# Performance work log

Measured on AMD Instinct MI355X. Metric: run time of the kernel, lower is better.

## Reference

```python
import jax, jax.numpy as jnp
import numpy as np

N_DETS = 16384
DEG = 32
E = N_DETS * DEG
NUM_BLOCKS = 4
SHORTCUT = 128   # shortcutDim
RED = 32         # reducedDim
INNER = 64       # blockInnerDim = 2*32
PW_IN = 9        # pwfeatRawInput
PW_HID = 256     # pwfeatInnerDim
PW_OUT = 32      # pwfeatOutDim


def _xavier(key, shape):
    fan_in, fan_out = shape[-2], shape[-1]
    lim = jnp.sqrt(6.0 / (fan_in + fan_out)).astype(jnp.float32)
    return jax.random.uniform(key, shape, jnp.float32, -lim, lim)


def setup_inputs() -> dict:
    key = jax.random.key(0)
    ks = jax.random.split(key, 24)
    inp = {}
    inp["detFeatures"] = jnp.zeros((N_DETS, SHORTCUT), jnp.float32)
    inp["pairRaw"] = jax.random.normal(ks[0], (E, PW_IN), jnp.float32)
    # every detection has DEG neighbor rows (sorted, all segments non-empty)
    inp["cIdxs"] = jnp.repeat(jnp.arange(N_DETS, dtype=jnp.int32), DEG)
    inp["nIdxs"] = jax.random.randint(ks[1], (E,), 0, N_DETS, jnp.int32)
    # pairwise-feature generator MLP: 9 -> 256 -> 256 -> 32
    inp["g_W1"] = _xavier(ks[2], (PW_IN, PW_HID)); inp["g_b1"] = jnp.zeros((PW_HID,), jnp.float32)
    inp["g_W2"] = _xavier(ks[3], (PW_HID, PW_HID)); inp["g_b2"] = jnp.zeros((PW_HID,), jnp.float32)
    inp["g_W3"] = _xavier(ks[4], (PW_HID, PW_OUT)); inp["g_b3"] = jnp.zeros((PW_OUT,), jnp.float32)
    # per-block params, stacked along leading block dim
    inp["blk_fc1_W"] = _xavier(ks[5], (NUM_BLOCKS, SHORTCUT, RED)); inp["blk_fc1_b"] = jnp.zeros((NUM_BLOCKS, RED), jnp.float32)
    inp["blk_pw_W1"] = _xavier(ks[6], (NUM_BLOCKS, 3 * RED, INNER)); inp["blk_pw_b1"] = jnp.zeros((NUM_BLOCKS, INNER), jnp.float32)
    inp["blk_pw_W2"] = _xavier(ks[7], (NUM_BLOCKS, INNER, INNER)); inp["blk_pw_b2"] = jnp.zeros((NUM_BLOCKS, INNER), jnp.float32)
    inp["blk_post_W1"] = _xavier(ks[8], (NUM_BLOCKS, INNER, INNER)); inp["blk_post_b1"] = jnp.zeros((NUM_BLOCKS, INNER), jnp.float32)
    inp["blk_post_W2"] = _xavier(ks[9], (NUM_BLOCKS, INNER, INNER)); inp["blk_post_b2"] = jnp.zeros((NUM_BLOCKS, INNER), jnp.float32)
    inp["blk_out_W"] = _xavier(ks[10], (NUM_BLOCKS, INNER, SHORTCUT)); inp["blk_out_b"] = jnp.zeros((NUM_BLOCKS, SHORTCUT), jnp.float32)
    inp["s_W"] = _xavier(ks[11], (3, SHORTCUT, SHORTCUT)); inp["s_b"] = jnp.zeros((3, SHORTCUT), jnp.float32)
    inp["pred_W"] = _xavier(ks[12], (SHORTCUT, 1)); inp["pred_b"] = jnp.zeros((1,), jnp.float32)
    return inp


def reference(detFeatures, pairRaw, cIdxs, nIdxs,
              g_W1, g_b1, g_W2, g_b2, g_W3, g_b3,
              blk_fc1_W, blk_fc1_b, blk_pw_W1, blk_pw_b1, blk_pw_W2, blk_pw_b2,
              blk_post_W1, blk_post_b1, blk_post_W2, blk_post_b2,
              blk_out_W, blk_out_b, s_W, s_b, pred_W, pred_b):
    relu = jax.nn.relu
    n_dets = detFeatures.shape[0]
    num_blocks = blk_fc1_W.shape[0]
    # GNet.pairwiseFeaturesFC: pwfeat generator MLP on raw 9-d pair descriptors
    pair = relu(pairRaw @ g_W1 + g_b1)          # (E, 256)
    pair = relu(pair @ g_W2 + g_b2)             # (E, 256)
    pair = relu(pair @ g_W3 + g_b3)             # (E, 32)
    is_id = (cIdxs == nIdxs)[:, None]           # zero-out self-neighbor feats
    x = detFeatures                             # (N, 128)
    for b in range(num_blocks):                 # structurally distinct blocks
        f = relu(x @ blk_fc1_W[b] + blk_fc1_b[b])          # (N, 32)
        cF = f[cIdxs]                                       # (E, 32) gather
        nF = jnp.where(is_id, jnp.float32(0), f[nIdxs])     # (E, 32) gather
        h = jnp.concatenate([pair, cF, nF], axis=1)         # (E, 96)
        h = relu(h @ blk_pw_W1[b] + blk_pw_b1[b])           # (E, 64)
        h = relu(h @ blk_pw_W2[b] + blk_pw_b2[b])           # (E, 64)
        # per-detection max pooling over neighbor rows (segment-max)
        m = jax.ops.segment_max(h, cIdxs, num_segments=n_dets,
                                indices_are_sorted=True)    # (N, 64)
        m = relu(m @ blk_post_W1[b] + blk_post_b1[b])
        m = relu(m @ blk_post_W2[b] + blk_post_b2[b])
        x = relu(x + m @ blk_out_W[b] + blk_out_b[b])        # residual + relu
    for i in range(s_W.shape[0]):
        x = relu(x @ s_W[i] + s_b[i])
    scores = (x @ pred_W + pred_b).reshape(-1)               # (N,)
    return scores
```

## Files before the change

kernel.cpp:

```cpp
#include <hip/hip_runtime.h>

#define N_DETS 16384
#define DEG 32
#define E_EDGES (N_DETS * DEG)
#define EDGE_GRID 512

typedef __attribute__((ext_vector_type(8))) short bf16x8;
typedef __attribute__((ext_vector_type(4))) float f32x4;

__device__ __forceinline__ ushort f32_to_bf16(float v) {
  unsigned u = __float_as_uint(v);
  u += 0x7FFFu + ((u >> 16) & 1u);
  return (ushort)(u >> 16);
}
__device__ __forceinline__ float bf16_to_f32(ushort h) {
  return __uint_as_float((unsigned)h << 16);
}

__global__ __launch_bounds__(256) void split_w_kernel(
    const float* __restrict__ W, ushort* __restrict__ hi, ushort* __restrict__ lo, int N)
{
  const int n = blockIdx.x, k = threadIdx.x;
  const float v = W[(size_t)k * N + n];
  const ushort h = f32_to_bf16(v);
  const ushort l = f32_to_bf16(v - bf16_to_f32(h));
  hi[(size_t)n * 256 + k] = h;
  lo[(size_t)n * 256 + k] = l;
}

__global__ __launch_bounds__(256) void split_edge_w_kernel(
    const float* __restrict__ W1all, const float* __restrict__ W2all,
    ushort* __restrict__ w1h, ushort* __restrict__ w1l,
    ushort* __restrict__ w2h, ushort* __restrict__ w2l)
{
  const int b = blockIdx.x;
  const float* W1 = W1all + b * 6144;
  const float* W2 = W2all + b * 4096;
  for (int i = threadIdx.x; i < 6144; i += 256) {
    const int col = i / 96, k = i % 96;
    const float v = W1[k * 64 + col];
    const ushort h = f32_to_bf16(v);
    w1h[b * 6144 + col * 96 + k] = h;
    w1l[b * 6144 + col * 96 + k] = f32_to_bf16(v - bf16_to_f32(h));
  }
  for (int i = threadIdx.x; i < 4096; i += 256) {
    const int col = i >> 6, k = i & 63;
    const float v = W2[k * 64 + col];
    const ushort h = f32_to_bf16(v);
    w2h[b * 4096 + col * 64 + k] = h;
    w2l[b * 4096 + col * 64 + k] = f32_to_bf16(v - bf16_to_f32(h));
  }
}

__global__ __launch_bounds__(128) void split_score_w_kernel(
    const float* __restrict__ sW, ushort* __restrict__ hi, ushort* __restrict__ lo)
{
  const int layer = blockIdx.x >> 7, col = blockIdx.x & 127, k = threadIdx.x;
  const float v = sW[layer * 16384 + k * 128 + col];
  const ushort h = f32_to_bf16(v);
  hi[layer * 16384 + col * 128 + k] = h;
  lo[layer * 16384 + col * 128 + k] = f32_to_bf16(v - bf16_to_f32(h));
}

__global__ __launch_bounds__(256) void split_post_w_kernel(
    const float* __restrict__ poW1, const float* __restrict__ poW2,
    const float* __restrict__ outW, const float* __restrict__ fc1W,
    ushort* __restrict__ p1h, ushort* __restrict__ p1l,
    ushort* __restrict__ p2h, ushort* __restrict__ p2l,
    ushort* __restrict__ oh,  ushort* __restrict__ ol,
    ushort* __restrict__ fh,  ushort* __restrict__ fl)
{
  const int b = blockIdx.x;
  for (int i = threadIdx.x; i < 4096; i += 256) {
    const int col = i >> 6, k = i & 63;
    float v = poW1[b * 4096 + k * 64 + col];
    ushort h = f32_to_bf16(v);
    p1h[b * 4096 + col * 64 + k] = h;
    p1l[b * 4096 + col * 64 + k] = f32_to_bf16(v - bf16_to_f32(h));
    v = poW2[b * 4096 + k * 64 + col];
    h = f32_to_bf16(v);
    p2h[b * 4096 + col * 64 + k] = h;
    p2l[b * 4096 + col * 64 + k] = f32_to_bf16(v - bf16_to_f32(h));
  }
  for (int i = threadIdx.x; i < 8192; i += 256) {
    const int col = i >> 6, k = i & 63;
    const float v = outW[b * 8192 + k * 128 + col];
    const ushort h = f32_to_bf16(v);
    oh[b * 8192 + col * 64 + k] = h;
    ol[b * 8192 + col * 64 + k] = f32_to_bf16(v - bf16_to_f32(h));
  }
  for (int i = threadIdx.x; i < 4096; i += 256) {
    const int col = i >> 7, k = i & 127;
    const float v = fc1W[b * 4096 + k * 32 + col];
    const ushort h = f32_to_bf16(v);
    fh[b * 4096 + col * 128 + k] = h;
    fl[b * 4096 + col * 128 + k] = f32_to_bf16(v - bf16_to_f32(h));
  }
}

#define A_STRIDE 264

__global__ __launch_bounds__(1024, 4) void pair_mlp_kernel(
    const float* __restrict__ raw,
    const float* __restrict__ W1, const float* __restrict__ b1,
    const ushort* __restrict__ w2h, const ushort* __restrict__ w2l,
    const float* __restrict__ b2,
    const ushort* __restrict__ w3h, const ushort* __restrict__ w3l,
    const float* __restrict__ b3,
    ushort* __restrict__ pair_h, ushort* __restrict__ pair_l)
{
  __shared__ __align__(16) ushort ah[64 * A_STRIDE];
  __shared__ __align__(16) ushort al[64 * A_STRIDE];
  __shared__ __align__(16) ushort w3sh[32 * A_STRIDE];
  __shared__ __align__(16) ushort w3sl[32 * A_STRIDE];
  __shared__ __align__(16) float rawt[64 * 12];

  const int t = threadIdx.x;
  const int lane = t & 63, wv = t >> 6;
  const int ln = lane & 15, kg = lane >> 4;

  for (int i = t; i < 32 * 64; i += 1024) {
    const int row = (i * 4) >> 8, col = (i * 4) & 255;
    *(ushort4*)&w3sh[row * A_STRIDE + col] = *(const ushort4*)&w3h[row * 256 + col];
    *(ushort4*)&w3sl[row * A_STRIDE + col] = *(const ushort4*)&w3l[row * 256 + col];
  }

  bf16x8 b2hreg[8], b2lreg[8];
  #pragma unroll
  for (int ks = 0; ks < 8; ++ks) {
    const size_t bo = (size_t)(wv * 16 + ln) * 256 + ks * 32 + kg * 8;
    b2hreg[ks] = *(const bf16x8*)&w2h[bo];
    b2lreg[ks] = *(const bf16x8*)&w2l[bo];
  }
  const float bias2 = b2[wv * 16 + ln];
  const int mt3 = (wv >> 1) & 3, nt3 = wv & 1;
  const float b3v = b3[nt3 * 16 + ln];
  __syncthreads();

  for (int grp = blockIdx.x; grp < E_EDGES / 64; grp += gridDim.x) {
    const long long e0 = (long long)grp * 64;

    if (t < 64 * 9) rawt[(t / 9) * 12 + (t % 9)] = raw[e0 * 9 + t];
    __syncthreads();

    {
      const int col = t & 255, r0 = (t >> 8) * 16;
      const float bv = b1[col];
      float wk[9];
      #pragma unroll
      for (int k = 0; k < 9; ++k) wk[k] = W1[k * 256 + col];
      #pragma unroll
      for (int r = 0; r < 16; ++r) {
        const int row = r0 + r;
        const float4 ra = *(const float4*)&rawt[row * 12];
        const float4 rb = *(const float4*)&rawt[row * 12 + 4];
        const float rc = rawt[row * 12 + 8];
        float s = bv;
        s = fmaf(ra.x, wk[0], s); s = fmaf(ra.y, wk[1], s);
        s = fmaf(ra.z, wk[2], s); s = fmaf(ra.w, wk[3], s);
        s = fmaf(rb.x, wk[4], s); s = fmaf(rb.y, wk[5], s);
        s = fmaf(rb.z, wk[6], s); s = fmaf(rb.w, wk[7], s);
        s = fmaf(rc, wk[8], s);
        const float v = fmaxf(s, 0.f);
        const ushort h = f32_to_bf16(v);
        ah[row * A_STRIDE + col] = h;
        al[row * A_STRIDE + col] = f32_to_bf16(v - bf16_to_f32(h));
      }
    }
    __syncthreads();

    f32x4 acc[4];
    #pragma unroll
    for (int mt = 0; mt < 4; ++mt) {
      acc[mt][0] = 0.f; acc[mt][1] = 0.f; acc[mt][2] = 0.f; acc[mt][3] = 0.f;
    }
    #pragma unroll
    for (int ks = 0; ks < 8; ++ks) {
      const int ka = ks * 32 + kg * 8;
      #pragma unroll
      for (int mt = 0; mt < 4; ++mt) {
        const bf16x8 ahf = *(const bf16x8*)&ah[(mt * 16 + ln) * A_STRIDE + ka];
        const bf16x8 alf = *(const bf16x8*)&al[(mt * 16 + ln) * A_STRIDE + ka];
        acc[mt] = __builtin_amdgcn_mfma_f32_16x16x32_bf16(ahf, b2hreg[ks], acc[mt], 0, 0, 0);
        acc[mt] = __builtin_amdgcn_mfma_f32_16x16x32_bf16(alf, b2hreg[ks], acc[mt], 0, 0, 0);
        acc[mt] = __builtin_amdgcn_mfma_f32_16x16x32_bf16(ahf, b2lreg[ks], acc[mt], 0, 0, 0);
      }
    }
    __syncthreads();

    {
      const int colg = wv * 16 + ln;
      #pragma unroll
      for (int mt = 0; mt < 4; ++mt)
        #pragma unroll
        for (int r = 0; r < 4; ++r) {
          const int rowe = mt * 16 + kg * 4 + r;
          const float v = fmaxf(acc[mt][r] + bias2, 0.f);
          const ushort h = f32_to_bf16(v);
          ah[rowe * A_STRIDE + colg] = h;
          al[rowe * A_STRIDE + colg] = f32_to_bf16(v - bf16_to_f32(h));
        }
    }
    __syncthreads();

    if (wv < 8) {
      f32x4 acc3;
      acc3[0] = 0.f; acc3[1] = 0.f; acc3[2] = 0.f; acc3[3] = 0.f;
      #pragma unroll
      for (int ks = 0; ks < 8; ++ks) {
        const int ka = ks * 32 + kg * 8;
        const bf16x8 a_h = *(const bf16x8*)&ah[(mt3 * 16 + ln) * A_STRIDE + ka];
        const bf16x8 a_l = *(const bf16x8*)&al[(mt3 * 16 + ln) * A_STRIDE + ka];
        const bf16x8 b_h = *(const bf16x8*)&w3sh[(nt3 * 16 + ln) * A_STRIDE + ka];
        const bf16x8 b_l = *(const bf16x8*)&w3sl[(nt3 * 16 + ln) * A_STRIDE + ka];
        acc3 = __builtin_amdgcn_mfma_f32_16x16x32_bf16(a_h, b_h, acc3, 0, 0, 0);
        acc3 = __builtin_amdgcn_mfma_f32_16x16x32_bf16(a_l, b_h, acc3, 0, 0, 0);
        acc3 = __builtin_amdgcn_mfma_f32_16x16x32_bf16(a_h, b_l, acc3, 0, 0, 0);
      }
      const int col3 = nt3 * 16 + ln;
      #pragma unroll
      for (int r = 0; r < 4; ++r) {
        const int rowe = mt3 * 16 + kg * 4 + r;
        const float v = fmaxf(acc3[r] + b3v, 0.f);
        const ushort h = f32_to_bf16(v);
        const size_t idx = (size_t)(e0 + rowe) * 32 + col3;
        pair_h[idx] = h;
        pair_l[idx] = f32_to_bf16(v - bf16_to_f32(h));
      }
    }
    __syncthreads();
  }
}

__global__ __launch_bounds__(256) void fc1_kernel(
    const float* __restrict__ x, const float* __restrict__ W,
    const float* __restrict__ b, float* __restrict__ f,
    ushort* __restrict__ f_h, ushort* __restrict__ f_l)
{
  __shared__ float Wl[128 * 32];
  const int t = threadIdx.x;
  #pragma unroll
  for (int j = 0; j < 4; ++j) {
    const int off = t * 4 + j * 1024;
    *(float4*)&Wl[off] = *(const float4*)&W[off];
  }
  __syncthreads();
  const int c = t & 31, rr = t >> 5;
  const long long r = (long long)blockIdx.x * 8 + rr;
  const float* xr = x + r * 128;
  float acc = b[c];
  #pragma unroll 8
  for (int k = 0; k < 128; k += 4) {
    const float4 a = *(const float4*)&xr[k];
    acc = fmaf(a.x, Wl[(k + 0) * 32 + c], acc);
    acc = fmaf(a.y, Wl[(k + 1) * 32 + c], acc);
    acc = fmaf(a.z, Wl[(k + 2) * 32 + c], acc);
    acc = fmaf(a.w, Wl[(k + 3) * 32 + c], acc);
  }
  const float v = fmaxf(acc, 0.f);
  f[r * 32 + c] = v;
  const ushort h = f32_to_bf16(v);
  f_h[r * 32 + c] = h;
  f_l[r * 32 + c] = f32_to_bf16(v - bf16_to_f32(h));
}

#define W1S 104
#define W2S 72
#define CTS 36

__global__ __launch_bounds__(512, 2) void edge_kernel(
    const ushort* __restrict__ pair_h, const ushort* __restrict__ pair_l,
    const float* __restrict__ f,
    const ushort* __restrict__ f_h, const ushort* __restrict__ f_l,
    const int* __restrict__ nIdxs,
    const float* __restrict__ W1g, const float* __restrict__ bb1,
    const ushort* __restrict__ gw1h, const ushort* __restrict__ gw1l,
    const ushort* __restrict__ gw2h, const ushort* __restrict__ gw2l,
    const float* __restrict__ bb2,
    float* __restrict__ m)
{
  __shared__ __align__(16) ushort W1hS[64 * W1S], W1lS[64 * W1S];
  __shared__ __align__(16) ushort W2hS[64 * W2S], W2lS[64 * W2S];
  __shared__ __align__(16) float  W1cT[64 * CTS];
  __shared__ __align__(16) ushort h1h[8][32 * W2S], h1l[8][32 * W2S];

  const int t = threadIdx.x;
  const int lane = t & 63, wv = t >> 6;
  const int ln = lane & 15, kg = lane >> 4;

  for (int i = t; i < 1536; i += 512) {
    const int idx = i * 4, row = idx / 96, k = idx % 96;
    *(ushort4*)&W1hS[row * W1S + k] = *(const ushort4*)&gw1h[idx];
    *(ushort4*)&W1lS[row * W1S + k] = *(const ushort4*)&gw1l[idx];
  }
  for (int i = t; i < 1024; i += 512) {
    const int idx = i * 4, row = idx >> 6, k = idx & 63;
    *(ushort4*)&W2hS[row * W2S + k] = *(const ushort4*)&gw2h[idx];
    *(ushort4*)&W2lS[row * W2S + k] = *(const ushort4*)&gw2l[idx];
  }
  for (int i = t; i < 2048; i += 512) {
    const int col = i >> 5, j = i & 31;
    W1cT[col * CTS + j] = W1g[(32 + j) * 64 + col];
  }
  __syncthreads();

  for (int dg = blockIdx.x; dg < N_DETS / 8; dg += gridDim.x) {
    const int d = dg * 8 + wv;
    const long long e0 = (long long)d * 32;

    float cfs[4];
    {
      const float4 fv0 = *(const float4*)&f[(size_t)d * 32 + kg * 8];
      const float4 fv1 = *(const float4*)&f[(size_t)d * 32 + kg * 8 + 4];
      #pragma unroll
      for (int nt = 0; nt < 4; ++nt) {
        const int col = nt * 16 + ln;
        const float4 w0 = *(const float4*)&W1cT[col * CTS + kg * 8];
        const float4 w1 = *(const float4*)&W1cT[col * CTS + kg * 8 + 4];
        float s = fv0.x * w0.x + fv0.y * w0.y + fv0.z * w0.z + fv0.w * w0.w
                + fv1.x * w1.x + fv1.y * w1.y + fv1.z * w1.z + fv1.w * w1.w;
        s += __shfl_xor(s, 16);
        s += __shfl_xor(s, 32);
        cfs[nt] = s + bb1[col];
      }
    }

    f32x4 acc1[4][2];
    #pragma unroll
    for (int nt = 0; nt < 4; ++nt)
      #pragma unroll
      for (int mt = 0; mt < 2; ++mt) {
        acc1[nt][mt][0] = 0.f; acc1[nt][mt][1] = 0.f;
        acc1[nt][mt][2] = 0.f; acc1[nt][mt][3] = 0.f;
      }
    bf16x8 ph[2], pl_[2], nh[2], nl_[2];
    #pragma unroll
    for (int mt = 0; mt < 2; ++mt) {
      const long long row = e0 + mt * 16 + ln;
      ph[mt]  = *(const bf16x8*)&pair_h[row * 32 + kg * 8];
      pl_[mt] = *(const bf16x8*)&pair_l[row * 32 + kg * 8];
      const int n = nIdxs[row];
      bf16x8 vh = *(const bf16x8*)&f_h[(size_t)n * 32 + kg * 8];
      bf16x8 vl = *(const bf16x8*)&f_l[(size_t)n * 32 + kg * 8];
      if (n == d) { vh = (bf16x8){0,0,0,0,0,0,0,0}; vl = (bf16x8){0,0,0,0,0,0,0,0}; }
      nh[mt] = vh; nl_[mt] = vl;
    }
    #pragma unroll
    for (int nt = 0; nt < 4; ++nt) {
      const int bro = (nt * 16 + ln) * W1S;
      const bf16x8 b0h = *(const bf16x8*)&W1hS[bro + kg * 8];
      const bf16x8 b0l = *(const bf16x8*)&W1lS[bro + kg * 8];
      const bf16x8 b1h = *(const bf16x8*)&W1hS[bro + 64 + kg * 8];
      const bf16x8 b1l = *(const bf16x8*)&W1lS[bro + 64 + kg * 8];
      #pragma unroll
      for (int mt = 0; mt < 2; ++mt) {
        acc1[nt][mt] = __builtin_amdgcn_mfma_f32_16x16x32_bf16(ph[mt], b0h, acc1[nt][mt], 0, 0, 0);
        acc1[nt][mt] = __builtin_amdgcn_mfma_f32_16x16x32_bf16(pl_[mt], b0h, acc1[nt][mt], 0, 0, 0);
        acc1[nt][mt] = __builtin_amdgcn_mfma_f32_16x16x32_bf16(ph[mt], b0l, acc1[nt][mt], 0, 0, 0);
        acc1[nt][mt] = __builtin_amdgcn_mfma_f32_16x16x32_bf16(nh[mt], b1h, acc1[nt][mt], 0, 0, 0);
        acc1[nt][mt] = __builtin_amdgcn_mfma_f32_16x16x32_bf16(nl_[mt], b1h, acc1[nt][mt], 0, 0, 0);
        acc1[nt][mt] = __builtin_amdgcn_mfma_f32_16x16x32_bf16(nh[mt], b1l, acc1[nt][mt], 0, 0, 0);
      }
    }

    #pragma unroll
    for (int nt = 0; nt < 4; ++nt) {
      const int col = nt * 16 + ln;
      #pragma unroll
      for (int mt = 0; mt < 2; ++mt)
        #pragma unroll
        for (int r = 0; r < 4; ++r) {
          const int row = mt * 16 + kg * 4 + r;
          const float v = fmaxf(acc1[nt][mt][r] + cfs[nt], 0.f);
          const ushort h = f32_to_bf16(v);
          h1h[wv][row * W2S + col] = h;
          h1l[wv][row * W2S + col] = f32_to_bf16(v - bf16_to_f32(h));
        }
    }

    f32x4 acc2[4][2];
    #pragma unroll
    for (int mt = 0; mt < 4; ++mt)
      #pragma unroll
      for (int nt = 0; nt < 2; ++nt) {
        acc2[mt][nt][0] = 0.f; acc2[mt][nt][1] = 0.f;
        acc2[mt][nt][2] = 0.f; acc2[mt][nt][3] = 0.f;
      }
    #pragma unroll
    for (int ks = 0; ks < 2; ++ks) {
      const int ka = ks * 32 + kg * 8;
      bf16x8 bh[2], bl[2];
      #pragma unroll
      for (int nt = 0; nt < 2; ++nt) {
        bh[nt] = *(const bf16x8*)&h1h[wv][(nt * 16 + ln) * W2S + ka];
        bl[nt] = *(const bf16x8*)&h1l[wv][(nt * 16 + ln) * W2S + ka];
      }
      #pragma unroll
      for (int mt = 0; mt < 4; ++mt) {
        const bf16x8 a_h = *(const bf16x8*)&W2hS[(mt * 16 + ln) * W2S + ka];
        const bf16x8 a_l = *(const bf16x8*)&W2lS[(mt * 16 + ln) * W2S + ka];
        #pragma unroll
        for (int nt = 0; nt < 2; ++nt) {
          acc2[mt][nt] = __builtin_amdgcn_mfma_f32_16x16x32_bf16(a_h, bh[nt], acc2[mt][nt], 0, 0, 0);
          acc2[mt][nt] = __builtin_amdgcn_mfma_f32_16x16x32_bf16(a_h, bl[nt], acc2[mt][nt], 0, 0, 0);
          acc2[mt][nt] = __builtin_amdgcn_mfma_f32_16x16x32_bf16(a_l, bh[nt], acc2[mt][nt], 0, 0, 0);
        }
      }
    }

    #pragma unroll
    for (int mt = 0; mt < 4; ++mt)
      #pragma unroll
      for (int r = 0; r < 4; ++r) {
        float mx = fmaxf(acc2[mt][0][r], acc2[mt][1][r]);
        mx = fmaxf(mx, __shfl_xor(mx, 1));
        mx = fmaxf(mx, __shfl_xor(mx, 2));
        mx = fmaxf(mx, __shfl_xor(mx, 4));
        mx = fmaxf(mx, __shfl_xor(mx, 8));
        if (ln == mt * 4 + r) {
          const int outcol = mt * 16 + kg * 4 + r;
          m[(size_t)d * 64 + outcol] = fmaxf(mx + bb2[outcol], 0.f);
        }
      }
  }
}

#define PS 72
#define PXS 136

__global__ __launch_bounds__(512) void postfc1_kernel(
    const float* __restrict__ m, const float* __restrict__ x,
    const ushort* __restrict__ p1h, const ushort* __restrict__ p1l,
    const float* __restrict__ pob1,
    const ushort* __restrict__ p2h, const ushort* __restrict__ p2l,
    const float* __restrict__ pob2,
    const ushort* __restrict__ oh, const ushort* __restrict__ ol,
    const float* __restrict__ outb,
    const ushort* __restrict__ fch, const ushort* __restrict__ fcl,
    const float* __restrict__ fcb, int do_fc1,
    float* __restrict__ y,
    float* __restrict__ f, ushort* __restrict__ f_h, ushort* __restrict__ f_l)
{
  __shared__ __align__(16) ushort mh[32 * PS], ml[32 * PS];
  __shared__ __align__(16) ushort hh[32 * PS], hl[32 * PS];
  __shared__ __align__(16) ushort yh[32 * PXS], yl[32 * PXS];
  const int t = threadIdx.x;
  const int lane = t & 63, wv = t >> 6;
  const int ln = lane & 15, kg = lane >> 4;
  const long long r0 = (long long)blockIdx.x * 32;

  for (int i = t; i < 32 * 16; i += 512) {
    const int row = i >> 4, cq = (i & 15) * 4;
    const float4 v4 = *(const float4*)&m[(r0 + row) * 64 + cq];
    const float vv[4] = {v4.x, v4.y, v4.z, v4.w};
    #pragma unroll
    for (int j = 0; j < 4; ++j) {
      const ushort h = f32_to_bf16(vv[j]);
      mh[row * PS + cq + j] = h;
      ml[row * PS + cq + j] = f32_to_bf16(vv[j] - bf16_to_f32(h));
    }
  }
  __syncthreads();

  {
    const int mt = wv >> 2, nt = wv & 3, col = nt * 16 + ln;
    const ushort* bh = p1h + (size_t)col * 64;
    const ushort* bl = p1l + (size_t)col * 64;
    f32x4 acc; acc[0] = 0.f; acc[1] = 0.f; acc[2] = 0.f; acc[3] = 0.f;
    #pragma unroll
    for (int ks = 0; ks < 2; ++ks) {
      const int ka = ks * 32 + kg * 8;
      const bf16x8 a_h = *(const bf16x8*)&mh[(mt * 16 + ln) * PS + ka];
      const bf16x8 a_l = *(const bf16x8*)&ml[(mt * 16 + ln) * PS + ka];
      const bf16x8 b_h = *(const bf16x8*)&bh[ka];
      const bf16x8 b_l = *(const bf16x8*)&bl[ka];
      acc = __builtin_amdgcn_mfma_f32_16x16x32_bf16(a_h, b_h, acc, 0, 0, 0);
      acc = __builtin_amdgcn_mfma_f32_16x16x32_bf16(a_l, b_h, acc, 0, 0, 0);
      acc = __builtin_amdgcn_mfma_f32_16x16x32_bf16(a_h, b_l, acc, 0, 0, 0);
    }
    const float bias = pob1[col];
    #pragma unroll
    for (int r = 0; r < 4; ++r) {
      const int row = mt * 16 + kg * 4 + r;
      const float v = fmaxf(acc[r] + bias, 0.f);
      const ushort h = f32_to_bf16(v);
      hh[row * PS + col] = h;
      hl[row * PS + col] = f32_to_bf16(v - bf16_to_f32(h));
    }
  }
  __syncthreads();

  {
    const int mt = wv >> 2, nt = wv & 3, col = nt * 16 + ln;
    const ushort* bh = p2h + (size_t)col * 64;
    const ushort* bl = p2l + (size_t)col * 64;
    f32x4 acc; acc[0] = 0.f; acc[1] = 0.f; acc[2] = 0.f; acc[3] = 0.f;
    #pragma unroll
    for (int ks = 0; ks < 2; ++ks) {
      const int ka = ks * 32 + kg * 8;
      const bf16x8 a_h = *(const bf16x8*)&hh[(mt * 16 + ln) * PS + ka];
      const bf16x8 a_l = *(const bf16x8*)&hl[(mt * 16 + ln) * PS + ka];
      const bf16x8 b_h = *(const bf16x8*)&bh[ka];
      const bf16x8 b_l = *(const bf16x8*)&bl[ka];
      acc = __builtin_amdgcn_mfma_f32_16x16x32_bf16(a_h, b_h, acc, 0, 0, 0);
      acc = __builtin_amdgcn_mfma_f32_16x16x32_bf16(a_l, b_h, acc, 0, 0, 0);
      acc = __builtin_amdgcn_mfma_f32_16x16x32_bf16(a_h, b_l, acc, 0, 0, 0);
    }
    const float bias = pob2[col];
    __syncthreads();
    #pragma unroll
    for (int r = 0; r < 4; ++r) {
      const int row = mt * 16 + kg * 4 + r;
      const float v = fmaxf(acc[r] + bias, 0.f);
      const ushort h = f32_to_bf16(v);
      mh[row * PS + col] = h;
      ml[row * PS + col] = f32_to_bf16(v - bf16_to_f32(h));
    }
  }
  __syncthreads();

  {
    const int col = wv * 16 + ln;
    const ushort* bh = oh + (size_t)col * 64;
    const ushort* bl = ol + (size_t)col * 64;
    f32x4 acc[2];
    #pragma unroll
    for (int mt = 0; mt < 2; ++mt) {
      acc[mt][0] = 0.f; acc[mt][1] = 0.f; acc[mt][2] = 0.f; acc[mt][3] = 0.f;
    }
    #pragma unroll
    for (int ks = 0; ks < 2; ++ks) {
      const int ka = ks * 32 + kg * 8;
      const bf16x8 b_h = *(const bf16x8*)&bh[ka];
      const bf16x8 b_l = *(const bf16x8*)&bl[ka];
      #pragma unroll
      for (int mt = 0; mt < 2; ++mt) {
        const bf16x8 a_h = *(const bf16x8*)&mh[(mt * 16 + ln) * PS + ka];
        const bf16x8 a_l = *(const bf16x8*)&ml[(mt * 16 + ln) * PS + ka];
        acc[mt] = __builtin_amdgcn_mfma_f32_16x16x32_bf16(a_h, b_h, acc[mt], 0, 0, 0);
        acc[mt] = __builtin_amdgcn_mfma_f32_16x16x32_bf16(a_l, b_h, acc[mt], 0, 0, 0);
        acc[mt] = __builtin_amdgcn_mfma_f32_16x16x32_bf16(a_h, b_l, acc[mt], 0, 0, 0);
      }
    }
    const float bias = outb[col];
    #pragma unroll
    for (int mt = 0; mt < 2; ++mt)
      #pragma unroll
      for (int r = 0; r < 4; ++r) {
        const int row = mt * 16 + kg * 4 + r;
        const size_t idx = (size_t)(r0 + row) * 128 + col;
        const float v = fmaxf(x[idx] + acc[mt][r] + bias, 0.f);
        y[idx] = v;
        const ushort h = f32_to_bf16(v);
        yh[row * PXS + col] = h;
        yl[row * PXS + col] = f32_to_bf16(v - bf16_to_f32(h));
      }
  }
  __syncthreads();

  if (do_fc1 && wv < 4) {
    const int mt = wv >> 1, nt = wv & 1, col = nt * 16 + ln;
    const ushort* bh = fch + (size_t)col * 128;
    const ushort* bl = fcl + (size_t)col * 128;
    f32x4 acc; acc[0] = 0.f; acc[1] = 0.f; acc[2] = 0.f; acc[3] = 0.f;
    #pragma unroll
    for (int ks = 0; ks < 4; ++ks) {
      const int ka = ks * 32 + kg * 8;
      const bf16x8 a_h = *(const bf16x8*)&yh[(mt * 16 + ln) * PXS + ka];
      const bf16x8 a_l = *(const bf16x8*)&yl[(mt * 16 + ln) * PXS + ka];
      const bf16x8 b_h = *(const bf16x8*)&bh[ka];
      const bf16x8 b_l = *(const bf16x8*)&bl[ka];
      acc = __builtin_amdgcn_mfma_f32_16x16x32_bf16(a_h, b_h, acc, 0, 0, 0);
      acc = __builtin_amdgcn_mfma_f32_16x16x32_bf16(a_l, b_h, acc, 0, 0, 0);
      acc = __builtin_amdgcn_mfma_f32_16x16x32_bf16(a_h, b_l, acc, 0, 0, 0);
    }
    const float bias = fcb[col];
    #pragma unroll
    for (int r = 0; r < 4; ++r) {
      const int row = mt * 16 + kg * 4 + r;
      const float v = fmaxf(acc[r] + bias, 0.f);
      const size_t idx = (size_t)(r0 + row) * 32 + col;
      f[idx] = v;
      const ushort h = f32_to_bf16(v);
      f_h[idx] = h;
      f_l[idx] = f32_to_bf16(v - bf16_to_f32(h));
    }
  }
}

#define XS 136

__global__ __launch_bounds__(512) void score_head_kernel(
    const float* __restrict__ x,
    const ushort* __restrict__ swh, const ushort* __restrict__ swl,
    const float* __restrict__ sb,
    const float* __restrict__ pW, const float* __restrict__ pb,
    float* __restrict__ out)
{
  __shared__ __align__(16) ushort xh[2][32 * XS], xl[2][32 * XS];
  __shared__ __align__(16) float hsf[32 * XS];
  __shared__ float pWs[128];
  const int t = threadIdx.x;
  const int lane = t & 63, wv = t >> 6;
  const int ln = lane & 15, kg = lane >> 4;
  const long long r0 = (long long)blockIdx.x * 32;

  if (t < 128) pWs[t] = pW[t];
  for (int i = t; i < 32 * 32; i += 512) {
    const int row = i >> 5, cq = (i & 31) * 4;
    const float4 v4 = *(const float4*)&x[(r0 + row) * 128 + cq];
    const float vv[4] = {v4.x, v4.y, v4.z, v4.w};
    #pragma unroll
    for (int j = 0; j < 4; ++j) {
      const ushort h = f32_to_bf16(vv[j]);
      xh[0][row * XS + cq + j] = h;
      xl[0][row * XS + cq + j] = f32_to_bf16(vv[j] - bf16_to_f32(h));
    }
  }
  __syncthreads();

  const int colg = wv * 16 + ln;
  int cur = 0;
  #pragma unroll 1
  for (int layer = 0; layer < 3; ++layer) {
    const ushort* wh = swh + (size_t)layer * 16384 + (size_t)colg * 128;
    const ushort* wl = swl + (size_t)layer * 16384 + (size_t)colg * 128;
    f32x4 acc[2];
    #pragma unroll
    for (int mt = 0; mt < 2; ++mt) {
      acc[mt][0] = 0.f; acc[mt][1] = 0.f; acc[mt][2] = 0.f; acc[mt][3] = 0.f;
    }
    #pragma unroll
    for (int ks = 0; ks < 4; ++ks) {
      const int ka = ks * 32 + kg * 8;
      const bf16x8 b_h = *(const bf16x8*)&wh[ka];
      const bf16x8 b_l = *(const bf16x8*)&wl[ka];
      #pragma unroll
      for (int mt = 0; mt < 2; ++mt) {
        const bf16x8 a_h = *(const bf16x8*)&xh[cur][(mt * 16 + ln) * XS + ka];
        const bf16x8 a_l = *(const bf16x8*)&xl[cur][(mt * 16 + ln) * XS + ka];
        acc[mt] = __builtin_amdgcn_mfma_f32_16x16x32_bf16(a_h, b_h, acc[mt], 0, 0, 0);
        acc[mt] = __builtin_amdgcn_mfma_f32_16x16x32_bf16(a_l, b_h, acc[mt], 0, 0, 0);
        acc[mt] = __builtin_amdgcn_mfma_f32_16x16x32_bf16(a_h, b_l, acc[mt], 0, 0, 0);
      }
    }
    const float bias = sb[layer * 128 + colg];
    __syncthreads();
    if (layer < 2) {
      #pragma unroll
      for (int mt = 0; mt < 2; ++mt)
        #pragma unroll
        for (int r = 0; r < 4; ++r) {
          const int row = mt * 16 + kg * 4 + r;
          const float v = fmaxf(acc[mt][r] + bias, 0.f);
          const ushort h = f32_to_bf16(v);
          xh[cur ^ 1][row * XS + colg] = h;
          xl[cur ^ 1][row * XS + colg] = f32_to_bf16(v - bf16_to_f32(h));
        }
      cur ^= 1;
    } else {
      #pragma unroll
      for (int mt = 0; mt < 2; ++mt)
        #pragma unroll
        for (int r = 0; r < 4; ++r) {
          const int row = mt * 16 + kg * 4 + r;
          hsf[row * XS + colg] = fmaxf(acc[mt][r] + bias, 0.f);
        }
    }
    __syncthreads();
  }

  {
    const int row = t >> 4, l16 = t & 15;
    const float4 a0 = *(const float4*)&hsf[row * XS + l16 * 8];
    const float4 a1 = *(const float4*)&hsf[row * XS + l16 * 8 + 4];
    const float4 w0 = *(const float4*)&pWs[l16 * 8];
    const float4 w1 = *(const float4*)&pWs[l16 * 8 + 4];
    float s = a0.x * w0.x + a0.y * w0.y + a0.z * w0.z + a0.w * w0.w
            + a1.x * w1.x + a1.y * w1.y + a1.z * w1.z + a1.w * w1.w;
    s += __shfl_xor(s, 1);
    s += __shfl_xor(s, 2);
    s += __shfl_xor(s, 4);
    s += __shfl_xor(s, 8);
    if (l16 == 0) out[r0 + row] = s + pb[0];
  }
}

extern "C" void kernel_launch(void* const* d_in, const int* in_sizes, int n_in,
                              void* d_out, int out_size, void* d_ws, size_t ws_size,
                              hipStream_t stream)
{
  const float* detF    = (const float*)d_in[0];
  const float* pairRaw = (const float*)d_in[1];
  const int*   cIdx    = (const int*)d_in[2];
  const int*   nIdx    = (const int*)d_in[3];
  const float* gW1 = (const float*)d_in[4];   const float* gb1 = (const float*)d_in[5];
  const float* gW2 = (const float*)d_in[6];   const float* gb2 = (const float*)d_in[7];
  const float* gW3 = (const float*)d_in[8];   const float* gb3 = (const float*)d_in[9];
  const float* fc1W = (const float*)d_in[10]; const float* fc1b = (const float*)d_in[11];
  const float* pwW1 = (const float*)d_in[12]; const float* pwb1 = (const float*)d_in[13];
  const float* pwW2 = (const float*)d_in[14]; const float* pwb2 = (const float*)d_in[15];
  const float* poW1 = (const float*)d_in[16]; const float* pob1 = (const float*)d_in[17];
  const float* poW2 = (const float*)d_in[18]; const float* pob2 = (const float*)d_in[19];
  const float* outW = (const float*)d_in[20]; const float* outb = (const float*)d_in[21];
  const float* sW = (const float*)d_in[22];   const float* sb = (const float*)d_in[23];
  const float* predW = (const float*)d_in[24]; const float* predb = (const float*)d_in[25];
  float* out = (float*)d_out;
  (void)cIdx;

  ushort* w2h  = (ushort*)d_ws;
  ushort* w2l  = w2h + 65536;
  ushort* w3h  = w2l + 65536;
  ushort* w3l  = w3h + 8192;
  ushort* w1eh = w3l + 8192;
  ushort* w1el = w1eh + 24576;
  ushort* w2eh = w1el + 24576;
  ushort* w2el = w2eh + 16384;
  ushort* swh  = w2el + 16384;
  ushort* swl  = swh + 49152;
  ushort* p1h  = swl + 49152;
  ushort* p1l  = p1h + 16384;
  ushort* p2h  = p1l + 16384;
  ushort* p2l  = p2h + 16384;
  ushort* ohh  = p2l + 16384;
  ushort* ohl  = ohh + 32768;
  ushort* fth  = ohl + 32768;
  ushort* ftl  = fth + 16384;
  ushort* pair_h = ftl + 16384;
  ushort* pair_l = pair_h + (size_t)E_EDGES * 32;
  ushort* f_h    = pair_l + (size_t)E_EDGES * 32;
  ushort* f_l    = f_h + (size_t)N_DETS * 32;
  float* f  = (float*)(f_l + (size_t)N_DETS * 32);
  float* m  = f  + (size_t)N_DETS * 32;
  float* xa = m  + (size_t)N_DETS * 64;
  float* xb = xa + (size_t)N_DETS * 128;

  hipMemcpyAsync(xa, detF, (size_t)N_DETS * 128 * sizeof(float),
                 hipMemcpyDeviceToDevice, stream);

  split_w_kernel<<<256, 256, 0, stream>>>(gW2, w2h, w2l, 256);
  split_w_kernel<<<32, 256, 0, stream>>>(gW3, w3h, w3l, 32);
  split_edge_w_kernel<<<4, 256, 0, stream>>>(pwW1, pwW2, w1eh, w1el, w2eh, w2el);
  split_score_w_kernel<<<384, 128, 0, stream>>>(sW, swh, swl);
  split_post_w_kernel<<<4, 256, 0, stream>>>(poW1, poW2, outW, fc1W,
      p1h, p1l, p2h, p2l, ohh, ohl, fth, ftl);

  pair_mlp_kernel<<<256, 1024, 0, stream>>>(pairRaw, gW1, gb1,
      w2h, w2l, gb2, w3h, w3l, gb3, pair_h, pair_l);

  fc1_kernel<<<N_DETS / 8, 256, 0, stream>>>(xa, fc1W, fc1b, f, f_h, f_l);

  float* xin = xa;
  float* xout = xb;
  for (int b = 0; b < 4; ++b) {
    edge_kernel<<<EDGE_GRID, 512, 0, stream>>>(pair_h, pair_l, f, f_h, f_l, nIdx,
        pwW1 + b * 6144, pwb1 + b * 64,
        w1eh + b * 6144, w1el + b * 6144, w2eh + b * 4096, w2el + b * 4096,
        pwb2 + b * 64, m);
    const int nb = (b + 1) & 3;
    postfc1_kernel<<<N_DETS / 32, 512, 0, stream>>>(m, xin,
        p1h + b * 4096, p1l + b * 4096, pob1 + b * 64,
        p2h + b * 4096, p2l + b * 4096, pob2 + b * 64,
        ohh + b * 8192, ohl + b * 8192, outb + b * 128,
        fth + nb * 4096, ftl + nb * 4096, fc1b + nb * 32, (b < 3) ? 1 : 0,
        xout, f, f_h, f_l);
    float* tmp = xout; xout = xin; xin = tmp;
  }
  score_head_kernel<<<N_DETS / 32, 512, 0, stream>>>(xin, swh, swl, sb,
      predW, predb, out);
}
```

Baseline: 678.2 us.

## Fuse edge message kernel with post-MLP and next-block fc1 kernel

Merges the per-block edge MLP plus segment-max kernel with the post-MLP, residual and next fc1 kernel into one kernel that handles 32 detections per workgroup. The pooled features stay in shared memory as hi/lo bf16 instead of going through a global fp32 buffer, and one launch per block is dropped. The fc1 output is double-buffered, because neighbor gathers of the current features could otherwise race with writes of the next features. The cost is a large combined LDS footprint that limits occupancy, and a per-tile serialization of the edge and post phases, which removes the old persistent-grid overlap.

```diff
diff --git a/kernel.cpp b/kernel.cpp
--- a/kernel.cpp
+++ b/kernel.cpp
@@ -3,7 +3,6 @@
 #define N_DETS 16384
 #define DEG 32
 #define E_EDGES (N_DETS * DEG)
-#define EDGE_GRID 512
 
 typedef __attribute__((ext_vector_type(8))) short bf16x8;
 typedef __attribute__((ext_vector_type(4))) float f32x4;
@@ -267,8 +266,9 @@
 #define W1S 104
 #define W2S 72
 #define CTS 36
-
-__global__ __launch_bounds__(512, 2) void edge_kernel(
+#define PXS 136
+
+__global__ __launch_bounds__(512, 2) void edge_post_kernel(
     const ushort* __restrict__ pair_h, const ushort* __restrict__ pair_l,
     const float* __restrict__ f,
     const ushort* __restrict__ f_h, const ushort* __restrict__ f_l,
@@ -277,16 +277,37 @@
     const ushort* __restrict__ gw1h, const ushort* __restrict__ gw1l,
     const ushort* __restrict__ gw2h, const ushort* __restrict__ gw2l,
     const float* __restrict__ bb2,
-    float* __restrict__ m)
-{
-  __shared__ __align__(16) ushort W1hS[64 * W1S], W1lS[64 * W1S];
-  __shared__ __align__(16) ushort W2hS[64 * W2S], W2lS[64 * W2S];
-  __shared__ __align__(16) float  W1cT[64 * CTS];
-  __shared__ __align__(16) ushort h1h[8][32 * W2S], h1l[8][32 * W2S];
+    const float* __restrict__ x,
+    const ushort* __restrict__ p1h, const ushort* __restrict__ p1l,
+    const float* __restrict__ pob1,
+    const ushort* __restrict__ p2h, const ushort* __restrict__ p2l,
+    const float* __restrict__ pob2,
+    const ushort* __restrict__ oh, const ushort* __restrict__ ol,
+    const float* __restrict__ outb,
+    const ushort* __restrict__ fch, const ushort* __restrict__ fcl,
+    const float* __restrict__ fcb, int do_fc1,
+    float* __restrict__ y,
+    float* __restrict__ fo, ushort* __restrict__ fo_h, ushort* __restrict__ fo_l)
+{
+  __shared__ __align__(16) unsigned char smem[137216];
+  ushort* W1hS = (ushort*)(smem);
+  ushort* W1lS = (ushort*)(smem + 13312);
+  ushort* W2hS = (ushort*)(smem + 26624);
+  ushort* W2lS = (ushort*)(smem + 35840);
+  float*  W1cT = (float*)(smem + 45056);
+  ushort* msh  = (ushort*)(smem + 54272);
+  ushort* msl  = (ushort*)(smem + 58880);
+  ushort* h1hB = (ushort*)(smem + 63488);
+  ushort* h1lB = (ushort*)(smem + 100352);
+  ushort* hhB  = (ushort*)(smem + 63488);
+  ushort* hlB  = (ushort*)(smem + 68096);
+  ushort* yhB  = (ushort*)(smem + 72704);
+  ushort* ylB  = (ushort*)(smem + 81408);
 
   const int t = threadIdx.x;
   const int lane = t & 63, wv = t >> 6;
   const int ln = lane & 15, kg = lane >> 4;
+  const long long r0 = (long long)blockIdx.x * 32;
 
   for (int i = t; i < 1536; i += 512) {
     const int idx = i * 4, row = idx / 96, k = idx % 96;
@@ -304,9 +325,14 @@
   }
   __syncthreads();
 
-  for (int dg = blockIdx.x; dg < N_DETS / 8; dg += gridDim.x) {
-    const int d = dg * 8 + wv;
+  ushort* h1h = h1hB + wv * 32 * W2S;
+  ushort* h1l = h1lB + wv * 32 * W2S;
+
+  #pragma unroll 1
+  for (int it = 0; it < 4; ++it) {
+    const int d = (int)r0 + it * 8 + wv;
     const long long e0 = (long long)d * 32;
+    const int rowt = it * 8 + wv;
 
     float cfs[4];
     {
@@ -373,8 +399,8 @@
           const int row = mt * 16 + kg * 4 + r;
           const float v = fmaxf(acc1[nt][mt][r] + cfs[nt], 0.f);
           const ushort h = f32_to_bf16(v);
-          h1h[wv][row * W2S + col] = h;
-          h1l[wv][row * W2S + col] = f32_to_bf16(v - bf16_to_f32(h));
+          h1h[row * W2S + col] = h;
+          h1l[row * W2S + col] = f32_to_bf16(v - bf16_to_f32(h));
         }
     }
 
@@ -392,8 +418,8 @@
       bf16x8 bh[2], bl[2];
       #pragma unroll
       for (int nt = 0; nt < 2; ++nt) {
-        bh[nt] = *(const bf16x8*)&h1h[wv][(nt * 16 + ln) * W2S + ka];
-        bl[nt] = *(const bf16x8*)&h1l[wv][(nt * 16 + ln) * W2S + ka];
+        bh[nt] = *(const bf16x8*)&h1h[(nt * 16 + ln) * W2S + ka];
+        bl[nt] = *(const bf16x8*)&h1l[(nt * 16 + ln) * W2S + ka];
       }
       #pragma unroll
       for (int mt = 0; mt < 4; ++mt) {
@@ -419,46 +445,12 @@
         mx = fmaxf(mx, __shfl_xor(mx, 8));
         if (ln == mt * 4 + r) {
           const int outcol = mt * 16 + kg * 4 + r;
-          m[(size_t)d * 64 + outcol] = fmaxf(mx + bb2[outcol], 0.f);
+          const float v = fmaxf(mx + bb2[outcol], 0.f);
+          const ushort h = f32_to_bf16(v);
+          msh[rowt * W2S + outcol] = h;
+          msl[rowt * W2S + outcol] = f32_to_bf16(v - bf16_to_f32(h));
         }
       }
-  }
-}
-
-#define PS 72
-#define PXS 136
-
-__global__ __launch_bounds__(512) void postfc1_kernel(
-    const float* __restrict__ m, const float* __restrict__ x,
-    const ushort* __restrict__ p1h, const ushort* __restrict__ p1l,
-    const float* __restrict__ pob1,
-    const ushort* __restrict__ p2h, const ushort* __restrict__ p2l,
-    const float* __restrict__ pob2,
-    const ushort* __restrict__ oh, const ushort* __restrict__ ol,
-    const float* __restrict__ outb,
-    const ushort* __restrict__ fch, const ushort* __restrict__ fcl,
-    const float* __restrict__ fcb, int do_fc1,
-    float* __restrict__ y,
-    float* __restrict__ f, ushort* __restrict__ f_h, ushort* __restrict__ f_l)
-{
-  __shared__ __align__(16) ushort mh[32 * PS], ml[32 * PS];
-  __shared__ __align__(16) ushort hh[32 * PS], hl[32 * PS];
-  __shared__ __align__(16) ushort yh[32 * PXS], yl[32 * PXS];
-  const int t = threadIdx.x;
-  const int lane = t & 63, wv = t >> 6;
-  const int ln = lane & 15, kg = lane >> 4;
-  const long long r0 = (long long)blockIdx.x * 32;
-
-  for (int i = t; i < 32 * 16; i += 512) {
-    const int row = i >> 4, cq = (i & 15) * 4;
-    const float4 v4 = *(const float4*)&m[(r0 + row) * 64 + cq];
-    const float vv[4] = {v4.x, v4.y, v4.z, v4.w};
-    #pragma unroll
-    for (int j = 0; j < 4; ++j) {
-      const ushort h = f32_to_bf16(vv[j]);
-      mh[row * PS + cq + j] = h;
-      ml[row * PS + cq + j] = f32_to_bf16(vv[j] - bf16_to_f32(h));
-    }
   }
   __syncthreads();
 
@@ -470,8 +462,8 @@
     #pragma unroll
     for (int ks = 0; ks < 2; ++ks) {
       const int ka = ks * 32 + kg * 8;
-      const bf16x8 a_h = *(const bf16x8*)&mh[(mt * 16 + ln) * PS + ka];
-      const bf16x8 a_l = *(const bf16x8*)&ml[(mt * 16 + ln) * PS + ka];
+      const bf16x8 a_h = *(const bf16x8*)&msh[(mt * 16 + ln) * W2S + ka];
+      const bf16x8 a_l = *(const bf16x8*)&msl[(mt * 16 + ln) * W2S + ka];
       const bf16x8 b_h = *(const bf16x8*)&bh[ka];
       const bf16x8 b_l = *(const bf16x8*)&bl[ka];
       acc = __builtin_amdgcn_mfma_f32_16x16x32_bf16(a_h, b_h, acc, 0, 0, 0);
@@ -484,8 +476,8 @@
       const int row = mt * 16 + kg * 4 + r;
       const float v = fmaxf(acc[r] + bias, 0.f);
       const ushort h = f32_to_bf16(v);
-      hh[row * PS + col] = h;
-      hl[row * PS + col] = f32_to_bf16(v - bf16_to_f32(h));
+      hhB[row * W2S + col] = h;
+      hlB[row * W2S + col] = f32_to_bf16(v - bf16_to_f32(h));
     }
   }
   __syncthreads();
@@ -498,8 +490,8 @@
     #pragma unroll
     for (int ks = 0; ks < 2; ++ks) {
       const int ka = ks * 32 + kg * 8;
-      const bf16x8 a_h = *(const bf16x8*)&hh[(mt * 16 + ln) * PS + ka];
-      const bf16x8 a_l = *(const bf16x8*)&hl[(mt * 16 + ln) * PS + ka];
+      const bf16x8 a_h = *(const bf16x8*)&hhB[(mt * 16 + ln) * W2S + ka];
+      const bf16x8 a_l = *(const bf16x8*)&hlB[(mt * 16 + ln) * W2S + ka];
       const bf16x8 b_h = *(const bf16x8*)&bh[ka];
       const bf16x8 b_l = *(const bf16x8*)&bl[ka];
       acc = __builtin_amdgcn_mfma_f32_16x16x32_bf16(a_h, b_h, acc, 0, 0, 0);
@@ -513,8 +505,8 @@
       const int row = mt * 16 + kg * 4 + r;
       const float v = fmaxf(acc[r] + bias, 0.f);
       const ushort h = f32_to_bf16(v);
-      mh[row * PS + col] = h;
-      ml[row * PS + col] = f32_to_bf16(v - bf16_to_f32(h));
+      msh[row * W2S + col] = h;
+      msl[row * W2S + col] = f32_to_bf16(v - bf16_to_f32(h));
     }
   }
   __syncthreads();
@@ -535,8 +527,8 @@
       const bf16x8 b_l = *(const bf16x8*)&bl[ka];
       #pragma unroll
       for (int mt = 0; mt < 2; ++mt) {
-        const bf16x8 a_h = *(const bf16x8*)&mh[(mt * 16 + ln) * PS + ka];
-        const bf16x8 a_l = *(const bf16x8*)&ml[(mt * 16 + ln) * PS + ka];
+        const bf16x8 a_h = *(const bf16x8*)&msh[(mt * 16 + ln) * W2S + ka];
+        const bf16x8 a_l = *(const bf16x8*)&msl[(mt * 16 + ln) * W2S + ka];
         acc[mt] = __builtin_amdgcn_mfma_f32_16x16x32_bf16(a_h, b_h, acc[mt], 0, 0, 0);
         acc[mt] = __builtin_amdgcn_mfma_f32_16x16x32_bf16(a_l, b_h, acc[mt], 0, 0, 0);
         acc[mt] = __builtin_amdgcn_mfma_f32_16x16x32_bf16(a_h, b_l, acc[mt], 0, 0, 0);
@@ -552,8 +544,8 @@
         const float v = fmaxf(x[idx] + acc[mt][r] + bias, 0.f);
         y[idx] = v;
         const ushort h = f32_to_bf16(v);
-        yh[row * PXS + col] = h;
-        yl[row * PXS + col] = f32_to_bf16(v - bf16_to_f32(h));
+        yhB[row * PXS + col] = h;
+        ylB[row * PXS + col] = f32_to_bf16(v - bf16_to_f32(h));
       }
   }
   __syncthreads();
@@ -566,8 +558,8 @@
     #pragma unroll
     for (int ks = 0; ks < 4; ++ks) {
       const int ka = ks * 32 + kg * 8;
-      const bf16x8 a_h = *(const bf16x8*)&yh[(mt * 16 + ln) * PXS + ka];
-      const bf16x8 a_l = *(const bf16x8*)&yl[(mt * 16 + ln) * PXS + ka];
+      const bf16x8 a_h = *(const bf16x8*)&yhB[(mt * 16 + ln) * PXS + ka];
+      const bf16x8 a_l = *(const bf16x8*)&ylB[(mt * 16 + ln) * PXS + ka];
       const bf16x8 b_h = *(const bf16x8*)&bh[ka];
       const bf16x8 b_l = *(const bf16x8*)&bl[ka];
       acc = __builtin_amdgcn_mfma_f32_16x16x32_bf16(a_h, b_h, acc, 0, 0, 0);
@@ -580,10 +572,10 @@
       const int row = mt * 16 + kg * 4 + r;
       const float v = fmaxf(acc[r] + bias, 0.f);
       const size_t idx = (size_t)(r0 + row) * 32 + col;
-      f[idx] = v;
+      fo[idx] = v;
       const ushort h = f32_to_bf16(v);
-      f_h[idx] = h;
-      f_l[idx] = f32_to_bf16(v - bf16_to_f32(h));
+      fo_h[idx] = h;
+      fo_l[idx] = f32_to_bf16(v - bf16_to_f32(h));
     }
   }
 }
@@ -728,11 +720,13 @@
   ushort* ftl  = fth + 16384;
   ushort* pair_h = ftl + 16384;
   ushort* pair_l = pair_h + (size_t)E_EDGES * 32;
-  ushort* f_h    = pair_l + (size_t)E_EDGES * 32;
-  ushort* f_l    = f_h + (size_t)N_DETS * 32;
-  float* f  = (float*)(f_l + (size_t)N_DETS * 32);
-  float* m  = f  + (size_t)N_DETS * 32;
-  float* xa = m  + (size_t)N_DETS * 64;
+  ushort* fA_h   = pair_l + (size_t)E_EDGES * 32;
+  ushort* fA_l   = fA_h + (size_t)N_DETS * 32;
+  ushort* fB_h   = fA_l + (size_t)N_DETS * 32;
+  ushort* fB_l   = fB_h + (size_t)N_DETS * 32;
+  float* fA = (float*)(fB_l + (size_t)N_DETS * 32);
+  float* fB = fA + (size_t)N_DETS * 32;
+  float* xa = fB + (size_t)N_DETS * 32;
   float* xb = xa + (size_t)N_DETS * 128;
 
   hipMemcpyAsync(xa, detF, (size_t)N_DETS * 128 * sizeof(float),
@@ -748,23 +742,29 @@
   pair_mlp_kernel<<<256, 1024, 0, stream>>>(pairRaw, gW1, gb1,
       w2h, w2l, gb2, w3h, w3l, gb3, pair_h, pair_l);
 
-  fc1_kernel<<<N_DETS / 8, 256, 0, stream>>>(xa, fc1W, fc1b, f, f_h, f_l);
+  fc1_kernel<<<N_DETS / 8, 256, 0, stream>>>(xa, fc1W, fc1b, fA, fA_h, fA_l);
 
   float* xin = xa;
   float* xout = xb;
+  float* fin = fA;  ushort* finh = fA_h;  ushort* finl = fA_l;
+  float* fo  = fB;  ushort* foh  = fB_h;  ushort* fol  = fB_l;
   for (int b = 0; b < 4; ++b) {
-    edge_kernel<<<EDGE_GRID, 512, 0, stream>>>(pair_h, pair_l, f, f_h, f_l, nIdx,
+    const int nb = (b + 1) & 3;
+    edge_post_kernel<<<N_DETS / 32, 512, 0, stream>>>(pair_h, pair_l,
+        fin, finh, finl, nIdx,
         pwW1 + b * 6144, pwb1 + b * 64,
         w1eh + b * 6144, w1el + b * 6144, w2eh + b * 4096, w2el + b * 4096,
-        pwb2 + b * 64, m);
-    const int nb = (b + 1) & 3;
-    postfc1_kernel<<<N_DETS / 32, 512, 0, stream>>>(m, xin,
+        pwb2 + b * 64,
+        xin,
         p1h + b * 4096, p1l + b * 4096, pob1 + b * 64,
         p2h + b * 4096, p2l + b * 4096, pob2 + b * 64,
         ohh + b * 8192, ohl + b * 8192, outb + b * 128,
         fth + nb * 4096, ftl + nb * 4096, fc1b + nb * 32, (b < 3) ? 1 : 0,
-        xout, f, f_h, f_l);
+        xout, fo, foh, fol);
     float* tmp = xout; xout = xin; xin = tmp;
+    float* tf = fo; fo = fin; fin = tf;
+    ushort* th = foh; foh = finh; finh = th;
+    ushort* tl = fol; fol = finl; finl = tl;
   }
   score_head_kernel<<<N_DETS / 32, 512, 0, stream>>>(xin, swh, swl, sb,
       predW, predb, out);
```

Result: no change. 672.2 us, median of 2 (-0.9%).
